# Performance work log

Hardware: AMD Instinct MI355X
Metric: run time of the kernel (lower is better)

## Reference

```python
import jax, jax.numpy as jnp
import numpy as np

N = 50000   # nodes
E = 800000  # edges (before self-loops)


def _gcn_conv(X, W, b, src, dst, dinv, n):
    # PyG GCNConv: out[i] = sum_j norm_ij * (X W)[j] + b, norm_ij = d_i^-1/2 d_j^-1/2
    h = X @ W                                   # [N, d_out]
    norm = dinv[src] * dinv[dst]                # [E+N]
    msg = h[src] * norm[:, None]                # gather + scale
    return jax.ops.segment_sum(msg, dst, num_segments=n) + b


def setup_inputs() -> dict:
    key = jax.random.key(0)
    k1, k2, k3, k4 = jax.random.split(key, 4)
    X = jax.random.normal(k1, (N, 128), dtype=jnp.float32)
    edge_index = jax.random.randint(k2, (2, E), 0, N, dtype=jnp.int64)
    W1 = jax.random.normal(k3, (128, 128), dtype=jnp.float32) * (1.0 / np.sqrt(128))
    b1 = jnp.zeros((128,), jnp.float32)
    W2 = jax.random.normal(k4, (128, 64), dtype=jnp.float32) * (1.0 / np.sqrt(128))
    b2 = jnp.zeros((64,), jnp.float32)
    return {"X": X, "edge_index": edge_index, "W1": W1, "b1": b1, "W2": W2, "b2": b2}


def reference(X, edge_index, W1, b1, W2, b2):
    n = X.shape[0]
    loops = jnp.arange(n, dtype=edge_index.dtype)
    src = jnp.concatenate([edge_index[0], loops])   # A + I
    dst = jnp.concatenate([edge_index[1], loops])
    deg = jax.ops.segment_sum(jnp.ones(src.shape[0], X.dtype), dst, num_segments=n)
    dinv = jnp.where(deg > 0, jax.lax.rsqrt(deg), 0.0)

    h = _gcn_conv(X, W1, b1, src, dst, dinv, n)                     # gcn1
    h = jax.nn.relu(_gcn_conv(h, W1, b1, src, dst, dinv, n))        # gcn1 again (as in source), relu
    # dropout: eval mode (identity)
    logits = _gcn_conv(h, W2, b2, src, dst, dinv, n)                # gcn2
    return jax.nn.log_softmax(logits, axis=1)
```

## Files before the change

kernel.cpp:

```cpp
#include <hip/hip_runtime.h>
#include <hip/hip_fp16.h>
#include <type_traits>

typedef _Float16 f16x8 __attribute__((ext_vector_type(8)));
typedef float    f32x4 __attribute__((ext_vector_type(4)));

__device__ inline unsigned int pack2(float a, float b) {
    __half2 h = __floats2half2_rn(a, b);
    return *(unsigned int*)&h;
}
__device__ inline float2 unpack2(unsigned int u) {
    __half2 h = *(__half2*)&u;
    return __half22float2(h);
}

#define MAXB 8192


__global__ void zero_kernel(int* __restrict__ p, int len) {
    int i = blockIdx.x * blockDim.x + threadIdx.x;
    if (i < len) p[i] = 0;
}

__global__ __launch_bounds__(256) void bucket_scatter_kernel(
    const int* __restrict__ src, const int* __restrict__ dst, int E, int nbuck,
    int* __restrict__ bcursor, unsigned int* __restrict__ staging) {
    __shared__ int hist[256];
    __shared__ int base[256];
    const int t = threadIdx.x;
    const int chunk = (E + gridDim.x - 1) / gridDim.x;
    const int e0 = blockIdx.x * chunk;
    const int e1 = min(E, e0 + chunk);
    for (int i = t; i < nbuck; i += 256) hist[i] = 0;
    __syncthreads();
    for (int e = e0 + t; e < e1; e += 256)
        atomicAdd(&hist[((unsigned)dst[e]) >> 8], 1);
    __syncthreads();
    for (int i = t; i < nbuck; i += 256) {
        int c = hist[i];
        base[i] = (c > 0) ? atomicAdd(&bcursor[i], c) : 0;
        hist[i] = 0;
    }
    __syncthreads();
    for (int e = e0 + t; e < e1; e += 256) {
        int d = dst[e];
        int b = ((unsigned)d) >> 8;
        int off = atomicAdd(&hist[b], 1);
        staging[(size_t)b * MAXB + base[b] + off] =
            (unsigned)src[e] | ((unsigned)(d & 255) << 16);
    }
}

__global__ __launch_bounds__(256) void bucket_hist_kernel(
    const unsigned int* __restrict__ staging, const int* __restrict__ bcursor,
    int n, int* __restrict__ counts, float* __restrict__ dinv,
    int* __restrict__ deghist) {
    __shared__ int hist[256];
    __shared__ int dh[256];
    const int b = blockIdx.x, t = threadIdx.x;
    hist[t] = 0;
    dh[t] = 0;
    __syncthreads();
    const int cnt = bcursor[b];
    const unsigned int* rec = staging + (size_t)b * MAXB;
    for (int i = t; i < cnt; i += 256) atomicAdd(&hist[(rec[i] >> 16) & 255], 1);
    __syncthreads();
    int node = (b << 8) + t;
    if (node < n) {
        int c = hist[t];
        counts[node] = c;
        dinv[node]   = rsqrtf(1.0f + (float)c);
        atomicAdd(&dh[min(c, 255)], 1);
    }
    __syncthreads();
    if (dh[t] > 0) atomicAdd(&deghist[t], dh[t]);
}

__global__ __launch_bounds__(256) void scan_small_kernel(const int* __restrict__ in,
                                                         int* __restrict__ out, int nb) {
    __shared__ int s[256];
    int t = threadIdx.x;
    int v = (t < nb) ? in[t] : 0;
    s[t] = v;
    __syncthreads();
    for (int off = 1; off < 256; off <<= 1) {
        int u = (t >= off) ? s[t - off] : 0;
        __syncthreads();
        s[t] += u;
        __syncthreads();
    }
    if (t < nb) out[t] = s[t] - v;
}

__global__ __launch_bounds__(256) void scan_write_kernel(const int* __restrict__ counts,
                                                         const int* __restrict__ blockoff, int n,
                                                         int* __restrict__ rowptr) {
    __shared__ int s[256];
    int t = threadIdx.x;
    int i = blockIdx.x * 256 + t;
    int v = (i < n) ? counts[i] : 0;
    s[t] = v;
    __syncthreads();
    for (int off = 1; off < 256; off <<= 1) {
        int u = (t >= off) ? s[t - off] : 0;
        __syncthreads();
        s[t] += u;
        __syncthreads();
    }
    int excl = blockoff[blockIdx.x] + s[t] - v;
    if (i < n) {
        rowptr[i] = excl;
        if (i == n - 1) rowptr[n] = excl + v;
    }
}

__global__ __launch_bounds__(256) void perm_kernel(const int* __restrict__ counts,
                                                   int* __restrict__ degoff, int n,
                                                   int* __restrict__ perm) {
    __shared__ int dh[256];
    __shared__ int dbase[256];
    const int t = threadIdx.x;
    const int i = blockIdx.x * 256 + t;
    dh[t] = 0;
    __syncthreads();
    int c = 0;
    const bool v = (i < n);
    if (v) {
        c = min(counts[i], 255);
        atomicAdd(&dh[c], 1);
    }
    __syncthreads();
    int h = dh[t];
    dbase[t] = (h > 0) ? atomicAdd(&degoff[t], h) : 0;
    dh[t] = 0;
    __syncthreads();
    if (v) {
        int off = atomicAdd(&dh[c], 1);
        perm[dbase[c] + off] = i;
    }
}

__global__ __launch_bounds__(256) void bucket_place_kernel(
    const unsigned int* __restrict__ staging, const int* __restrict__ bcursor,
    const int* __restrict__ rowptr, int n, unsigned short* __restrict__ edges) {
    __shared__ int lcur[256];
    const int b = blockIdx.x, t = threadIdx.x;
    int node = (b << 8) + t;
    lcur[t] = rowptr[min(node, n)];
    __syncthreads();
    const int cnt = bcursor[b];
    const unsigned int* rec = staging + (size_t)b * MAXB;
    for (int i = t; i < cnt; i += 256) {
        unsigned r = rec[i];
        int dl = (r >> 16) & 255;
        int p  = atomicAdd(&lcur[dl], 1);
        edges[p] = (unsigned short)(r & 0xffffu);
    }
}

template <int DOUT, typename TIN>
__global__ __launch_bounds__(256) void gemm_mfma(const TIN* __restrict__ A,
                                                 const float* __restrict__ W,
                                                 const float* __restrict__ dinv,
                                                 __half* __restrict__ C, int n) {
    constexpr int NF = DOUT / 16;
    __shared__ __align__(16) unsigned char wlds[DOUT * 256];

    const int t = threadIdx.x;
    for (int p = t; p < 64 * DOUT; p += 256) {
        int nn = p % DOUT;
        int k  = (p / DOUT) * 2;
        float w0 = W[(size_t)k * DOUT + nn];
        float w1 = W[(size_t)(k + 1) * DOUT + nn];
        int byte = (nn * 256 + k * 2) ^ ((nn & 7) << 4);
        *(unsigned int*)(wlds + byte) = pack2(w0, w1);
    }
    __syncthreads();

    const int w  = t >> 6;
    const int l  = t & 63;
    const int m  = (blockIdx.x * 4 + w) * 16 + (l & 15);
    const int kq = l >> 4;
    const bool valid = (m < n);

    f32x4 acc[NF];
#pragma unroll
    for (int i = 0; i < NF; ++i) acc[i] = (f32x4){0.f, 0.f, 0.f, 0.f};

#pragma unroll
    for (int ks = 0; ks < 4; ++ks) {
        const int k0 = ks * 32 + kq * 8;
        f16x8 af = {0, 0, 0, 0, 0, 0, 0, 0};
        if (valid) {
            if constexpr (std::is_same<TIN, float>::value) {
                const float4 x0 = *(const float4*)&A[(size_t)m * 128 + k0];
                const float4 x1 = *(const float4*)&A[(size_t)m * 128 + k0 + 4];
                af[0] = (_Float16)x0.x; af[1] = (_Float16)x0.y;
                af[2] = (_Float16)x0.z; af[3] = (_Float16)x0.w;
                af[4] = (_Float16)x1.x; af[5] = (_Float16)x1.y;
                af[6] = (_Float16)x1.z; af[7] = (_Float16)x1.w;
            } else {
                af = *(const f16x8*)&A[(size_t)m * 128 + k0];
            }
        }
#pragma unroll
        for (int nf = 0; nf < NF; ++nf) {
            int nn = nf * 16 + (l & 15);
            int byte = (nn * 256 + k0 * 2) ^ ((nn & 7) << 4);
            f16x8 bf = *(const f16x8*)(wlds + byte);
            acc[nf] = __builtin_amdgcn_mfma_f32_16x16x32_f16(bf, af, acc[nf], 0, 0, 0);
        }
    }

    if (valid) {
        const float di = dinv[m];
#pragma unroll
        for (int nf = 0; nf < NF; ++nf) {
            uint2 o;
            o.x = pack2(di * acc[nf][0], di * acc[nf][1]);
            o.y = pack2(di * acc[nf][2], di * acc[nf][3]);
            *(uint2*)&C[(size_t)m * DOUT + nf * 16 + kq * 4] = o;
        }
    }
}

template <int DOUT, bool RELU, bool LSM, typename TOUT>
__global__ __launch_bounds__(256) void agg_kernel(const __half* __restrict__ H,
                                                  const int* __restrict__ rowptr,
                                                  const unsigned short* __restrict__ edges,
                                                  const int* __restrict__ perm,
                                                  const float* __restrict__ dinv,
                                                  const float* __restrict__ bias,
                                                  TOUT* __restrict__ out, int n) {
    constexpr int LPR = DOUT / 8;
    constexpr int RPB = 256 / LPR;
    const int rid  = blockIdx.x * RPB + threadIdx.x / LPR;
    const int lane = threadIdx.x % LPR;
    if (rid >= n) return;
    const int row = perm[rid];

    const uint4* Hv = (const uint4*)H;

    float a[8];
    {
        uint4 h = Hv[(size_t)row * LPR + lane];
        float2 f;
        f = unpack2(h.x); a[0] = f.x; a[1] = f.y;
        f = unpack2(h.y); a[2] = f.x; a[3] = f.y;
        f = unpack2(h.z); a[4] = f.x; a[5] = f.y;
        f = unpack2(h.w); a[6] = f.x; a[7] = f.y;
    }
    auto accum = [&](uint4 h) {
        float2 f;
        f = unpack2(h.x); a[0] += f.x; a[1] += f.y;
        f = unpack2(h.y); a[2] += f.x; a[3] += f.y;
        f = unpack2(h.z); a[4] += f.x; a[5] += f.y;
        f = unpack2(h.w); a[6] += f.x; a[7] += f.y;
    };

    int j        = rowptr[row];
    const int je = rowptr[row + 1];
    for (; j + 1 < je; j += 2) {
        int s0 = edges[j];
        int s1 = edges[j + 1];
        uint4 h0 = Hv[(size_t)s0 * LPR + lane];
        uint4 h1 = Hv[(size_t)s1 * LPR + lane];
        accum(h0);
        accum(h1);
    }
    if (j < je) accum(Hv[(size_t)edges[j] * LPR + lane]);

    const float di = dinv[row];
    const float4 b0 = ((const float4*)bias)[lane * 2];
    const float4 b1 = ((const float4*)bias)[lane * 2 + 1];
    a[0] = b0.x + di * a[0]; a[1] = b0.y + di * a[1];
    a[2] = b0.z + di * a[2]; a[3] = b0.w + di * a[3];
    a[4] = b1.x + di * a[4]; a[5] = b1.y + di * a[5];
    a[6] = b1.z + di * a[6]; a[7] = b1.w + di * a[7];

    if (RELU) {
#pragma unroll
        for (int i = 0; i < 8; ++i) a[i] = fmaxf(a[i], 0.f);
    }

    if constexpr (LSM) {
        float m8 = a[0];
#pragma unroll
        for (int i = 1; i < 8; ++i) m8 = fmaxf(m8, a[i]);
#pragma unroll
        for (int off = 1; off < LPR; off <<= 1) m8 = fmaxf(m8, __shfl_xor(m8, off, LPR));
        float s = 0.f;
#pragma unroll
        for (int i = 0; i < 8; ++i) s += expf(a[i] - m8);
#pragma unroll
        for (int off = 1; off < LPR; off <<= 1) s += __shfl_xor(s, off, LPR);
        float ls = m8 + logf(s);
        float* op = (float*)out + (size_t)row * DOUT + lane * 8;
        *(float4*)op       = make_float4(a[0] - ls, a[1] - ls, a[2] - ls, a[3] - ls);
        *(float4*)(op + 4) = make_float4(a[4] - ls, a[5] - ls, a[6] - ls, a[7] - ls);
    } else {
        uint4 o;
        o.x = pack2(a[0], a[1]);
        o.y = pack2(a[2], a[3]);
        o.z = pack2(a[4], a[5]);
        o.w = pack2(a[6], a[7]);
        *(uint4*)&((__half*)out)[(size_t)row * DOUT + lane * 8] = o;
    }
}


extern "C" void kernel_launch(void* const* d_in, const int* in_sizes, int n_in,
                              void* d_out, int out_size, void* d_ws, size_t ws_size,
                              hipStream_t stream) {
    const float* X  = (const float*)d_in[0];
    const int*   ei = (const int*)d_in[1];
    const float* W1 = (const float*)d_in[2];
    const float* b1 = (const float*)d_in[3];
    const float* W2 = (const float*)d_in[4];
    const float* b2 = (const float*)d_in[5];

    const int n = in_sizes[0] / 128;
    const int E = in_sizes[1] / 2;
    const int* src = ei;
    const int* dst = ei + E;
    const int nbuck = (n + 255) >> 8;

    char* ws = (char*)d_ws;
    size_t off = 0;
    auto alloc = [&](size_t bytes) -> void* {
        void* p = ws + off;
        off = (off + bytes + 255) & ~(size_t)255;
        return p;
    };
    int*            zbuf    = (int*)  alloc((size_t)(nbuck + 256) * 4);
    int*            bcursor = zbuf;
    int*            deghist = zbuf + nbuck;
    float*          dinv    = (float*)alloc((size_t)n * 4);
    int*            counts  = (int*)  alloc((size_t)n * 4);
    int*            rowptr  = (int*)  alloc((size_t)(n + 1) * 4);
    int*            bexcl   = (int*)  alloc((size_t)nbuck * 4);
    int*            degoff  = (int*)  alloc(256 * 4);
    int*            perm    = (int*)  alloc((size_t)n * 4);
    unsigned int*   staging = (unsigned int*)alloc((size_t)nbuck * MAXB * 4);
    unsigned short* edges   = (unsigned short*)alloc((size_t)E * 2);
    __half*         P       = (__half*)alloc((size_t)n * 128 * 2);
    __half*         Q       = (__half*)alloc((size_t)n * 128 * 2);

    const int nb = (n + 255) / 256;

    zero_kernel<<<(nbuck + 256 + 255) / 256, 256, 0, stream>>>(zbuf, nbuck + 256);
    bucket_scatter_kernel<<<392, 256, 0, stream>>>(src, dst, E, nbuck, bcursor, staging);
    bucket_hist_kernel<<<nbuck, 256, 0, stream>>>(staging, bcursor, n, counts, dinv, deghist);
    scan_small_kernel<<<1, 256, 0, stream>>>(bcursor, bexcl, nbuck);
    scan_small_kernel<<<1, 256, 0, stream>>>(deghist, degoff, 256);
    scan_write_kernel<<<nb, 256, 0, stream>>>(counts, bexcl, n, rowptr);
    perm_kernel<<<nb, 256, 0, stream>>>(counts, degoff, n, perm);
    bucket_place_kernel<<<nbuck, 256, 0, stream>>>(staging, bcursor, rowptr, n, edges);

    const int gb = (n + 63) / 64;
    const int ab16 = (n + 15) / 16;
    const int ab32 = (n + 31) / 32;

    gemm_mfma<128, float><<<gb, 256, 0, stream>>>(X, W1, dinv, P, n);
    agg_kernel<128, false, false, __half><<<ab16, 256, 0, stream>>>(
        P, rowptr, edges, perm, dinv, b1, Q, n);

    gemm_mfma<128, __half><<<gb, 256, 0, stream>>>(Q, W1, dinv, P, n);
    agg_kernel<128, true, false, __half><<<ab16, 256, 0, stream>>>(
        P, rowptr, edges, perm, dinv, b1, Q, n);

    gemm_mfma<64, __half><<<gb, 256, 0, stream>>>(Q, W2, dinv, P, n);
    agg_kernel<64, false, true, float><<<ab32, 256, 0, stream>>>(
        P, rowptr, edges, perm, dinv, b2, (float*)d_out, n);
}
```

Measured before the change: 189.4 us.

## Split feature matrices into 32-column slabs so aggregation gathers fit in cache

The intermediate half-precision feature matrices now use a slab-major layout of 32-column quarters. The GEMMs write that layout and the aggregation kernel handles one slab per block, with block IDs interleaved so that consecutive blocks work on the same slab. The goal is to shrink the random-gather working set (n×32 halfs per slab) so it stays in L2/LLC rather than streaming the full rows. This costs re-reading rowptr, edges and perm once per slab, plus a separate log-softmax kernel because one row's features are now spread across blocks.

```diff
diff --git a/kernel.cpp b/kernel.cpp
--- a/kernel.cpp
+++ b/kernel.cpp
@@ -200,7 +200,7 @@
                 af[4] = (_Float16)x1.x; af[5] = (_Float16)x1.y;
                 af[6] = (_Float16)x1.z; af[7] = (_Float16)x1.w;
             } else {
-                af = *(const f16x8*)&A[(size_t)m * 128 + k0];
+                af = *(const f16x8*)&A[((size_t)ks * n + m) * 32 + kq * 8];
             }
         }
 #pragma unroll
@@ -219,12 +219,12 @@
             uint2 o;
             o.x = pack2(di * acc[nf][0], di * acc[nf][1]);
             o.y = pack2(di * acc[nf][2], di * acc[nf][3]);
-            *(uint2*)&C[(size_t)m * DOUT + nf * 16 + kq * 4] = o;
+            *(uint2*)&C[((size_t)(nf >> 1) * n + m) * 32 + (nf & 1) * 16 + kq * 4] = o;
         }
     }
 }
 
-template <int DOUT, bool RELU, bool LSM, typename TOUT>
+template <int NQ, bool RELU, typename TOUT>
 __global__ __launch_bounds__(256) void agg_kernel(const __half* __restrict__ H,
                                                   const int* __restrict__ rowptr,
                                                   const unsigned short* __restrict__ edges,
@@ -232,18 +232,22 @@
                                                   const float* __restrict__ dinv,
                                                   const float* __restrict__ bias,
                                                   TOUT* __restrict__ out, int n) {
-    constexpr int LPR = DOUT / 8;
-    constexpr int RPB = 256 / LPR;
-    const int rid  = blockIdx.x * RPB + threadIdx.x / LPR;
-    const int lane = threadIdx.x % LPR;
+    constexpr int SPQ = 8 / NQ;
+    const int bid = blockIdx.x;
+    const int xs  = bid & 7;
+    const int q   = xs / SPQ;
+    const int rg  = (bid >> 3) * SPQ + (xs % SPQ);
+    const int t   = threadIdx.x;
+    const int rid = rg * 64 + (t >> 2);
+    const int fl  = t & 3;
     if (rid >= n) return;
     const int row = perm[rid];
 
-    const uint4* Hv = (const uint4*)H;
+    const uint4* Hv = (const uint4*)(H + (size_t)q * n * 32);
 
     float a[8];
     {
-        uint4 h = Hv[(size_t)row * LPR + lane];
+        uint4 h = Hv[(size_t)row * 4 + fl];
         float2 f;
         f = unpack2(h.x); a[0] = f.x; a[1] = f.y;
         f = unpack2(h.y); a[2] = f.x; a[3] = f.y;
@@ -263,16 +267,16 @@
     for (; j + 1 < je; j += 2) {
         int s0 = edges[j];
         int s1 = edges[j + 1];
-        uint4 h0 = Hv[(size_t)s0 * LPR + lane];
-        uint4 h1 = Hv[(size_t)s1 * LPR + lane];
+        uint4 h0 = Hv[(size_t)s0 * 4 + fl];
+        uint4 h1 = Hv[(size_t)s1 * 4 + fl];
         accum(h0);
         accum(h1);
     }
-    if (j < je) accum(Hv[(size_t)edges[j] * LPR + lane]);
+    if (j < je) accum(Hv[(size_t)edges[j] * 4 + fl]);
 
     const float di = dinv[row];
-    const float4 b0 = ((const float4*)bias)[lane * 2];
-    const float4 b1 = ((const float4*)bias)[lane * 2 + 1];
+    const float4 b0 = *(const float4*)&bias[q * 32 + fl * 8];
+    const float4 b1 = *(const float4*)&bias[q * 32 + fl * 8 + 4];
     a[0] = b0.x + di * a[0]; a[1] = b0.y + di * a[1];
     a[2] = b0.z + di * a[2]; a[3] = b0.w + di * a[3];
     a[4] = b1.x + di * a[4]; a[5] = b1.y + di * a[5];
@@ -283,29 +287,33 @@
         for (int i = 0; i < 8; ++i) a[i] = fmaxf(a[i], 0.f);
     }
 
-    if constexpr (LSM) {
-        float m8 = a[0];
-#pragma unroll
-        for (int i = 1; i < 8; ++i) m8 = fmaxf(m8, a[i]);
-#pragma unroll
-        for (int off = 1; off < LPR; off <<= 1) m8 = fmaxf(m8, __shfl_xor(m8, off, LPR));
-        float s = 0.f;
-#pragma unroll
-        for (int i = 0; i < 8; ++i) s += expf(a[i] - m8);
-#pragma unroll
-        for (int off = 1; off < LPR; off <<= 1) s += __shfl_xor(s, off, LPR);
-        float ls = m8 + logf(s);
-        float* op = (float*)out + (size_t)row * DOUT + lane * 8;
-        *(float4*)op       = make_float4(a[0] - ls, a[1] - ls, a[2] - ls, a[3] - ls);
-        *(float4*)(op + 4) = make_float4(a[4] - ls, a[5] - ls, a[6] - ls, a[7] - ls);
-    } else {
+    if constexpr (std::is_same<TOUT, __half>::value) {
         uint4 o;
         o.x = pack2(a[0], a[1]);
         o.y = pack2(a[2], a[3]);
         o.z = pack2(a[4], a[5]);
         o.w = pack2(a[6], a[7]);
-        *(uint4*)&((__half*)out)[(size_t)row * DOUT + lane * 8] = o;
-    }
+        *(uint4*)&((__half*)out)[((size_t)q * n + row) * 32 + fl * 8] = o;
+    } else {
+        float* op = (float*)out + (size_t)row * (NQ * 32) + q * 32 + fl * 8;
+        *(float4*)op       = make_float4(a[0], a[1], a[2], a[3]);
+        *(float4*)(op + 4) = make_float4(a[4], a[5], a[6], a[7]);
+    }
+}
+
+__global__ __launch_bounds__(256) void logsoftmax_kernel(float* __restrict__ out, int n) {
+    int row  = blockIdx.x * 4 + (threadIdx.x >> 6);
+    int lane = threadIdx.x & 63;
+    if (row >= n) return;
+    float x = out[(size_t)row * 64 + lane];
+    float m = x;
+#pragma unroll
+    for (int off = 32; off >= 1; off >>= 1) m = fmaxf(m, __shfl_xor(m, off, 64));
+    float ex = expf(x - m);
+    float s  = ex;
+#pragma unroll
+    for (int off = 32; off >= 1; off >>= 1) s += __shfl_xor(s, off, 64);
+    out[(size_t)row * 64 + lane] = x - m - logf(s);
 }
 
 
@@ -357,19 +365,21 @@
     perm_kernel<<<nb, 256, 0, stream>>>(counts, degoff, n, perm);
     bucket_place_kernel<<<nbuck, 256, 0, stream>>>(staging, bcursor, rowptr, n, edges);
 
-    const int gb = (n + 63) / 64;
-    const int ab16 = (n + 15) / 16;
-    const int ab32 = (n + 31) / 32;
+    const int gb  = (n + 63) / 64;
+    const int rgs = (n + 63) / 64;
+    const int ab4 = 8 * ((rgs + 1) / 2);
+    const int ab2 = 8 * ((rgs + 3) / 4);
 
     gemm_mfma<128, float><<<gb, 256, 0, stream>>>(X, W1, dinv, P, n);
-    agg_kernel<128, false, false, __half><<<ab16, 256, 0, stream>>>(
+    agg_kernel<4, false, __half><<<ab4, 256, 0, stream>>>(
         P, rowptr, edges, perm, dinv, b1, Q, n);
 
     gemm_mfma<128, __half><<<gb, 256, 0, stream>>>(Q, W1, dinv, P, n);
-    agg_kernel<128, true, false, __half><<<ab16, 256, 0, stream>>>(
+    agg_kernel<4, true, __half><<<ab4, 256, 0, stream>>>(
         P, rowptr, edges, perm, dinv, b1, Q, n);
 
     gemm_mfma<64, __half><<<gb, 256, 0, stream>>>(Q, W2, dinv, P, n);
-    agg_kernel<64, false, true, float><<<ab32, 256, 0, stream>>>(
+    agg_kernel<2, false, float><<<ab2, 256, 0, stream>>>(
         P, rowptr, edges, perm, dinv, b2, (float*)d_out, n);
-}
+    logsoftmax_kernel<<<(n + 3) / 4, 256, 0, stream>>>((float*)d_out, n);
+}
```

Measured after the change: 210.5 us. +11.2%, slower.
